# Optimization experiments

Hardware: AMD Instinct MI355X
Metric: run time of the kernel (lower is better)

The kernel has to match this reference:

```python
import jax, jax.numpy as jnp
import numpy as np

B, E, H, W = 32, 512, 16, 16
NH, HD = 8, 64          # num_heads = embed_dim // num_heads_channels, head_dim = 64
OUT = 512
S = H * W + 1           # spacial_dim**2 + 1 = 257 (mean token prepended)


def setup_inputs() -> dict:
    key = jax.random.key(0)
    ks = jax.random.split(key, 10)
    sc = 1.0 / np.sqrt(E).astype(np.float32)
    n = lambda k, sh, s=1.0: jax.random.normal(k, sh, jnp.float32) * s
    return {
        "x_real": n(ks[0], (B, E, H, W)),
        "x_imag": n(ks[1], (B, E, H, W)),
        # positional_embedding = (randn/sqrt(E)).to(complex64) -> imag part is zero
        "pos_r": n(ks[2], (E, S), sc),
        "pos_i": jnp.zeros((E, S), jnp.float32),
        # complex in-projection (packed q,k,v) and out-projection of the MHA
        "w_in_r": n(ks[3], (3 * E, E), sc),
        "w_in_i": n(ks[4], (3 * E, E), sc),
        "b_in_r": jnp.zeros((3 * E,), jnp.float32),
        "b_in_i": jnp.zeros((3 * E,), jnp.float32),
        "w_out_r": n(ks[5], (E, E), sc),
        "w_out_i": n(ks[6], (E, E), sc),
        "b_out_r": jnp.zeros((E,), jnp.float32),
        "b_out_i": jnp.zeros((E,), jnp.float32),
        # complex 1x1 conv projection == complex linear over channels
        "w_p_r": n(ks[7], (OUT, E), sc),
        "w_p_i": n(ks[8], (OUT, E), sc),
        "b_p_r": jnp.zeros((OUT,), jnp.float32),
        "b_p_i": jnp.zeros((OUT,), jnp.float32),
    }


def _attention_pool(x_real, x_imag, pos_r, pos_i, w_in_r, w_in_i, b_in_r, b_in_i,
                    w_out_r, w_out_i, b_out_r, b_out_i, w_p_r, w_p_i, b_p_r, b_p_i):
    cx = jax.lax.complex
    x = cx(x_real, x_imag).reshape(B, E, -1)                       # [b,c,HW]
    x = jnp.concatenate([x.mean(-1, keepdims=True), x], axis=-1)   # [b,c,S]
    x = x + cx(pos_r, pos_i)[None]                                 # + pos embed
    x = x.transpose(0, 2, 1)                                       # [b,S,E]

    qkv = jnp.einsum('bse,fe->bsf', x, cx(w_in_r, w_in_i)) + cx(b_in_r, b_in_i)
    q, k, v = jnp.split(qkv, 3, axis=-1)
    q = q.reshape(B, S, NH, HD) / jnp.sqrt(jnp.float32(HD))
    k = k.reshape(B, S, NH, HD)
    v = v.reshape(B, S, NH, HD)

    logits = jnp.einsum('bqhd,bkhd->bhqk', q, k)                   # complex scores
    # complex softmax handled separately on real/imag parts
    w = cx(jax.nn.softmax(logits.real, axis=-1),
           jax.nn.softmax(logits.imag, axis=-1))
    attn = jnp.einsum('bhqk,bkhd->bqhd', w, v).reshape(B, S, E)
    attn = jnp.einsum('bse,fe->bsf', attn, cx(w_out_r, w_out_i)) + cx(b_out_r, b_out_i)

    y = attn.transpose(0, 2, 1)                                    # [b,E,S]
    y = jnp.einsum('oc,bcs->bos', cx(w_p_r, w_p_i), y) + cx(b_p_r, b_p_i)[None, :, None]
    return y[:, :, 0]                                              # [b,OUT] complex64


def reference(x_real, x_imag, pos_r, pos_i, w_in_r, w_in_i, b_in_r, b_in_i,
              w_out_r, w_out_i, b_out_r, b_out_i, w_p_r, w_p_i, b_p_r, b_p_i):
    return _attention_pool(x_real, x_imag, pos_r, pos_i, w_in_r, w_in_i, b_in_r,
                           b_in_i, w_out_r, w_out_i, b_out_r, b_out_i,
                           w_p_r, w_p_i, b_p_r, b_p_i)
```

## Files before the change

kernel.cpp:

```cpp
#include <hip/hip_runtime.h>

#define B_   32
#define E_   512
#define HW_  256
#define S_   257
#define NH_  8
#define NBLK 1024
#define NTHR 256
#define NGRP 32
#define GSZ  32
#define LG_  260

__device__ __forceinline__ void st_sys(float* p, float v) {
  __hip_atomic_store(p, v, __ATOMIC_RELAXED, __HIP_MEMORY_SCOPE_SYSTEM);
}
__device__ __forceinline__ void st_sys2(float2* p, float2 v) {
  unsigned long long u;
  __builtin_memcpy(&u, &v, 8);
  __hip_atomic_store((unsigned long long*)p, u, __ATOMIC_RELAXED, __HIP_MEMORY_SCOPE_SYSTEM);
}

__device__ __forceinline__ float wave_reduce(float v) {
  #pragma unroll
  for (int o = 32; o > 0; o >>= 1) v += __shfl_down(v, o, 64);
  return v;
}

__device__ __forceinline__ void gbar(unsigned* slots, int g, int j, int t, unsigned phase) {
  __syncthreads();
  if (t < 64) {
    if (t == 0)
      __hip_atomic_store(&slots[g * GSZ + j], phase, __ATOMIC_RELAXED, __HIP_MEMORY_SCOPE_SYSTEM);
    const unsigned* line = slots + g * GSZ;
    int sl = t & 31;
    for (;;) {
      unsigned v = __hip_atomic_load(&line[sl], __ATOMIC_RELAXED, __HIP_MEMORY_SCOPE_SYSTEM);
      if (__all((int)(v >= phase))) break;
      __builtin_amdgcn_s_sleep(2);
    }
  }
  __syncthreads();
}

__device__ void softmax257(float* l, float* red, int t) {
  int lane = t & 63, wv = t >> 6;
  float v = l[t];
  float v256 = l[256];
  float m = v;
  #pragma unroll
  for (int o = 32; o > 0; o >>= 1) m = fmaxf(m, __shfl_xor(m, o, 64));
  if (lane == 0) red[wv] = m;
  __syncthreads();
  float M = fmaxf(fmaxf(fmaxf(red[0], red[1]), fmaxf(red[2], red[3])), v256);
  float ex = expf(v - M);
  float e256 = expf(v256 - M);
  float s = ex;
  #pragma unroll
  for (int o = 32; o > 0; o >>= 1) s += __shfl_xor(s, o, 64);
  if (lane == 0) red[4 + wv] = s;
  __syncthreads();
  float inv = 1.f / (red[4] + red[5] + red[6] + red[7] + e256);
  l[t] = ex * inv;
  if (t == 0) l[256] = e256 * inv;
  __syncthreads();
}

__global__ __launch_bounds__(NTHR, 4) void k_mega(
    const float* __restrict__ xr, const float* __restrict__ xi,
    const float* __restrict__ pos_r, const float* __restrict__ pos_i,
    const float* __restrict__ w_in_r, const float* __restrict__ w_in_i,
    const float* __restrict__ b_in_r, const float* __restrict__ b_in_i,
    const float* __restrict__ w_out_r, const float* __restrict__ w_out_i,
    const float* __restrict__ b_out_r, const float* __restrict__ b_out_i,
    const float* __restrict__ w_p_r, const float* __restrict__ w_p_i,
    const float* __restrict__ b_p_r, const float* __restrict__ b_p_i,
    unsigned* slots,
    float* __restrict__ ur_, float* __restrict__ ui_,
    float* __restrict__ lgr, float* __restrict__ lgi,
    float* __restrict__ mr, float* __restrict__ mi,
    float* __restrict__ w2,
    float* __restrict__ zr_, float* __restrict__ zi_,
    float* __restrict__ a0r, float* __restrict__ a0i,
    float* __restrict__ aor, float* __restrict__ aoi,
    float* __restrict__ out, int interleaved) {
  __shared__ __align__(16) float smF[4112];
  const int t   = threadIdx.x;
  const int l   = t & 63;
  const int w   = t >> 6;
  const int bid = blockIdx.x;
  const int g   = bid >> 5;
  const int j   = bid & 31;

  #pragma unroll
  for (int rr = 0; rr < 4; ++rr) {
    int e = j * 16 + w * 4 + rr;
    float4 vr = ((const float4*)(xr + ((size_t)g * E_ + e) * HW_))[l];
    float4 vi = ((const float4*)(xi + ((size_t)g * E_ + e) * HW_))[l];
    float sr = (vr.x + vr.y) + (vr.z + vr.w);
    float si = (vi.x + vi.y) + (vi.z + vi.w);
    sr = wave_reduce(sr); si = wave_reduce(si);
    if (l == 0) {
      st_sys(&mr[g * E_ + e], sr * (1.f / HW_) + pos_r[(size_t)e * S_]);
      st_sys(&mi[g * E_ + e], si * (1.f / HW_) + pos_i[(size_t)e * S_]);
    }
  }
  gbar(slots, g, j, t, 1);

  {
    float* mR  = smF;
    float* mI  = smF + 512;
    float* q0L = smF + 1024;
    mR[t]       = mr[g * E_ + t];        mI[t]       = mi[g * E_ + t];
    mR[t + 256] = mr[g * E_ + t + 256];  mI[t + 256] = mi[g * E_ + t + 256];
    __syncthreads();
    #pragma unroll
    for (int rr = 0; rr < 4; ++rr) {
      int fl = w * 4 + rr;
      int f  = 16 * j + fl;
      const float* wr = w_in_r + (size_t)f * E_;
      const float* wi = w_in_i + (size_t)f * E_;
      float ar = 0.f, ai = 0.f;
      #pragma unroll
      for (int e = l; e < E_; e += 64) {
        float Xr = mR[e], Xi = mI[e], Cr = wr[e], Ci = wi[e];
        ar += Xr * Cr - Xi * Ci;
        ai += Xr * Ci + Xi * Cr;
      }
      ar = wave_reduce(ar); ai = wave_reduce(ai);
      if (l == 0) {
        q0L[fl * 2]     = (ar + b_in_r[f]) * 0.125f;
        q0L[fl * 2 + 1] = (ai + b_in_i[f]) * 0.125f;
      }
    }
    __syncthreads();
    int h = j >> 2;
    float u0r = 0.f, u0i = 0.f, u1r = 0.f, u1i = 0.f;
    #pragma unroll 4
    for (int fl = 0; fl < 16; ++fl) {
      int f = 16 * j + fl;
      float qr = q0L[fl * 2], qi = q0L[fl * 2 + 1];
      const float* Wr = w_in_r + (size_t)(E_ + f) * E_;
      const float* Wi = w_in_i + (size_t)(E_ + f) * E_;
      float W0r = Wr[t], W0i = Wi[t], W1r = Wr[t + 256], W1i = Wi[t + 256];
      u0r += qr * W0r - qi * W0i;  u0i += qr * W0i + qi * W0r;
      u1r += qr * W1r - qi * W1i;  u1i += qr * W1i + qi * W1r;
    }
    size_t ub = (size_t)(g * NH_ + h) * E_;
    atomicAdd(&ur_[ub + t], u0r);        atomicAdd(&ui_[ub + t], u0i);
    atomicAdd(&ur_[ub + t + 256], u1r);  atomicAdd(&ui_[ub + t + 256], u1i);
  }
  gbar(slots, g, j, t, 2);

  {
    int e0 = 16 * j;
    float* us = smF;
    if (t < 128) {
      int e = t & 15, hh = t >> 4;
      us[(e * 8 + hh) * 2]     = ur_[(size_t)(g * NH_ + hh) * E_ + e0 + e];
      us[(e * 8 + hh) * 2 + 1] = ui_[(size_t)(g * NH_ + hh) * E_ + e0 + e];
    }
    __syncthreads();
    float ar[NH_], ai[NH_];
    #pragma unroll
    for (int hh = 0; hh < NH_; ++hh) { ar[hh] = 0.f; ai[hh] = 0.f; }
    const float* xrb = xr + ((size_t)g * E_ + e0) * HW_;
    const float* xib = xi + ((size_t)g * E_ + e0) * HW_;
    #pragma unroll 2
    for (int e = 0; e < 16; ++e) {
      float Xr = xrb[e * HW_ + t] + pos_r[(size_t)(e0 + e) * S_ + t + 1];
      float Xi = xib[e * HW_ + t] + pos_i[(size_t)(e0 + e) * S_ + t + 1];
      #pragma unroll
      for (int hh = 0; hh < NH_; ++hh) {
        float Ur = us[(e * 8 + hh) * 2], Ui = us[(e * 8 + hh) * 2 + 1];
        ar[hh] += Xr * Ur - Xi * Ui;
        ai[hh] += Xr * Ui + Xi * Ur;
      }
    }
    #pragma unroll
    for (int hh = 0; hh < NH_; ++hh) {
      size_t lb = (size_t)(g * NH_ + hh) * LG_ + t + 1;
      atomicAdd(&lgr[lb], ar[hh]);
      atomicAdd(&lgi[lb], ai[hh]);
    }
  }
  gbar(slots, g, j, t, 3);

  if (j < NH_) {
    int bh = g * NH_ + j;
    float* lr  = smF;
    float* li  = smF + 260;
    float* redl = smF + 520;
    float* reds = smF + 528;
    lr[t + 1] = lgr[(size_t)bh * LG_ + t + 1];
    li[t + 1] = lgi[(size_t)bh * LG_ + t + 1];
    float pr = 0.f, pi = 0.f;
    #pragma unroll
    for (int e = t; e < E_; e += 256) {
      float Xr = mr[g * E_ + e], Xi = mi[g * E_ + e];
      float Ur = ur_[(size_t)bh * E_ + e], Ui = ui_[(size_t)bh * E_ + e];
      pr += Xr * Ur - Xi * Ui;
      pi += Xr * Ui + Xi * Ur;
    }
    pr = wave_reduce(pr); pi = wave_reduce(pi);
    if (l == 0) { redl[w * 2] = pr; redl[w * 2 + 1] = pi; }
    __syncthreads();
    if (t == 0) {
      lr[0] = redl[0] + redl[2] + redl[4] + redl[6];
      li[0] = redl[1] + redl[3] + redl[5] + redl[7];
    }
    __syncthreads();
    softmax257(lr, reds, t);
    softmax257(li, reds, t);
    float2* o = (float2*)w2 + (size_t)bh * S_;
    float2 v; v.x = lr[t]; v.y = li[t];
    st_sys2(&o[t], v);
    if (t == 0) { float2 v2; v2.x = lr[256]; v2.y = li[256]; st_sys2(&o[256], v2); }
  } else {
    int idx = t & 127;
    int e = 16 * j + (idx & 15);
    const float* src = (t < 128) ? xr : xi;
    float pf = src[((size_t)g * E_ + e) * HW_ + (idx >> 4) * 32];
    asm volatile("" :: "v"(pf));
  }
  gbar(slots, g, j, t, 4);

  {
    float2* wls = (float2*)smF;
    const float2* w2b = (const float2*)w2 + (size_t)g * NH_ * S_;
    for (int i = t; i < NH_ * S_; i += NTHR) wls[i] = w2b[i];
    __syncthreads();
    #pragma unroll
    for (int rr = 0; rr < 4; ++rr) {
      int e = 16 * j + 4 * w + rr;
      const float* xre = xr + ((size_t)g * E_ + e) * HW_;
      const float* xie = xi + ((size_t)g * E_ + e) * HW_;
      const float* pre = pos_r + (size_t)e * S_;
      const float* pie = pos_i + (size_t)e * S_;
      float ar2[NH_], ai2[NH_];
      #pragma unroll
      for (int hh = 0; hh < NH_; ++hh) { ar2[hh] = 0.f; ai2[hh] = 0.f; }
      #pragma unroll
      for (int jj = 0; jj < 4; ++jj) {
        int k = 1 + l + 64 * jj;
        float Xr = xre[k - 1] + pre[k];
        float Xi = xie[k - 1] + pie[k];
        #pragma unroll
        for (int hh = 0; hh < NH_; ++hh) {
          float2 W = wls[hh * S_ + k];
          ar2[hh] += W.x * Xr - W.y * Xi;
          ai2[hh] += W.x * Xi + W.y * Xr;
        }
      }
      #pragma unroll
      for (int hh = 0; hh < NH_; ++hh) { ar2[hh] = wave_reduce(ar2[hh]); ai2[hh] = wave_reduce(ai2[hh]); }
      if (l == 0) {
        float X0r = mr[g * E_ + e];
        float X0i = mi[g * E_ + e];
        #pragma unroll
        for (int hh = 0; hh < NH_; ++hh) {
          float2 W0 = wls[hh * S_];
          st_sys(&zr_[(size_t)(g * NH_ + hh) * E_ + e], ar2[hh] + W0.x * X0r - W0.y * X0i);
          st_sys(&zi_[(size_t)(g * NH_ + hh) * E_ + e], ai2[hh] + W0.x * X0i + W0.y * X0r);
        }
      }
    }
  }
  gbar(slots, g, j, t, 5);

  #pragma unroll
  for (int rr = 0; rr < 4; ++rr) {
    int f = j * 16 + w * 4 + rr;
    int h = f >> 6;
    const float* wrp = w_in_r + (size_t)(2 * E_ + f) * E_;
    const float* wip = w_in_i + (size_t)(2 * E_ + f) * E_;
    const float* zrp = zr_ + (size_t)(g * NH_ + h) * E_;
    const float* zip = zi_ + (size_t)(g * NH_ + h) * E_;
    float ar = 0.f, ai = 0.f;
    #pragma unroll
    for (int e = l; e < E_; e += 64) {
      float Zr = zrp[e], Zi = zip[e], Cr = wrp[e], Ci = wip[e];
      ar += Zr * Cr - Zi * Ci;
      ai += Zr * Ci + Zi * Cr;
    }
    ar = wave_reduce(ar); ai = wave_reduce(ai);
    if (l == 0) {
      float bvr = b_in_r[2 * E_ + f], bvi = b_in_i[2 * E_ + f];
      st_sys(&a0r[g * E_ + f], ar + (bvr - bvi));
      st_sys(&a0i[g * E_ + f], ai + (bvr + bvi));
    }
  }
  gbar(slots, g, j, t, 6);

  #pragma unroll
  for (int rr = 0; rr < 4; ++rr) {
    int f = j * 16 + w * 4 + rr;
    const float* wrp = w_out_r + (size_t)f * E_;
    const float* wip = w_out_i + (size_t)f * E_;
    const float* ir = a0r + (size_t)g * E_;
    const float* ii = a0i + (size_t)g * E_;
    float ar = 0.f, ai = 0.f;
    #pragma unroll
    for (int e = l; e < E_; e += 64) {
      float Xr = ir[e], Xi = ii[e], Cr = wrp[e], Ci = wip[e];
      ar += Xr * Cr - Xi * Ci;
      ai += Xr * Ci + Xi * Cr;
    }
    ar = wave_reduce(ar); ai = wave_reduce(ai);
    if (l == 0) { st_sys(&aor[g * E_ + f], ar + b_out_r[f]); st_sys(&aoi[g * E_ + f], ai + b_out_i[f]); }
  }
  gbar(slots, g, j, t, 7);

  #pragma unroll
  for (int rr = 0; rr < 4; ++rr) {
    int f = j * 16 + w * 4 + rr;
    const float* wrp = w_p_r + (size_t)f * E_;
    const float* wip = w_p_i + (size_t)f * E_;
    const float* ir = aor + (size_t)g * E_;
    const float* ii = aoi + (size_t)g * E_;
    float ar = 0.f, ai = 0.f;
    #pragma unroll
    for (int e = l; e < E_; e += 64) {
      float Xr = ir[e], Xi = ii[e], Cr = wrp[e], Ci = wip[e];
      ar += Xr * Cr - Xi * Ci;
      ai += Xr * Ci + Xi * Cr;
    }
    ar = wave_reduce(ar); ai = wave_reduce(ai);
    if (l == 0) {
      float rr2 = ar + b_p_r[f];
      float im  = ai + b_p_i[f];
      int wid = g * E_ + f;
      if (interleaved) { out[(size_t)wid * 2] = rr2; out[(size_t)wid * 2 + 1] = im; }
      else             { out[wid] = rr2; }
    }
  }
}

extern "C" void kernel_launch(void* const* d_in, const int* in_sizes, int n_in,
                              void* d_out, int out_size, void* d_ws, size_t ws_size,
                              hipStream_t stream) {
  (void)in_sizes; (void)n_in; (void)ws_size;
  const float* xr      = (const float*)d_in[0];
  const float* xi      = (const float*)d_in[1];
  const float* pos_r   = (const float*)d_in[2];
  const float* pos_i   = (const float*)d_in[3];
  const float* w_in_r  = (const float*)d_in[4];
  const float* w_in_i  = (const float*)d_in[5];
  const float* b_in_r  = (const float*)d_in[6];
  const float* b_in_i  = (const float*)d_in[7];
  const float* w_out_r = (const float*)d_in[8];
  const float* w_out_i = (const float*)d_in[9];
  const float* b_out_r = (const float*)d_in[10];
  const float* b_out_i = (const float*)d_in[11];
  const float* w_p_r   = (const float*)d_in[12];
  const float* w_p_i   = (const float*)d_in[13];
  const float* b_p_r   = (const float*)d_in[14];
  const float* b_p_i   = (const float*)d_in[15];

  const int BE = B_ * E_, BHE = B_ * NH_ * E_;
  float* ws = (float*)d_ws;
  unsigned* slots = (unsigned*)d_ws;
  float* ur   = ws + 1024;
  float* ui   = ur + BHE;
  float* lgr  = ui + BHE;
  float* lgi  = lgr + B_ * NH_ * LG_;
  float* mr   = lgi + B_ * NH_ * LG_;
  float* mi   = mr + BE;
  float* w2   = mi + BE;
  float* zr   = w2 + (size_t)2 * B_ * NH_ * S_;
  float* zi   = zr + BHE;
  float* a0r  = zi + BHE;
  float* a0i  = a0r + BE;
  float* aor  = a0i + BE;
  float* aoi  = aor + BE;

  size_t zbytes = (size_t)(1024 + 2 * BHE + 2 * B_ * NH_ * LG_) * 4;
  hipMemsetAsync(d_ws, 0, zbytes, stream);
  k_mega<<<NBLK, NTHR, 0, stream>>>(
      xr, xi, pos_r, pos_i, w_in_r, w_in_i, b_in_r, b_in_i,
      w_out_r, w_out_i, b_out_r, b_out_i, w_p_r, w_p_i, b_p_r, b_p_i,
      slots, ur, ui, lgr, lgi, mr, mi, w2, zr, zi, a0r, a0i, aor, aoi,
      (float*)d_out, out_size >= 2 * B_ * E_);
}
```

Before: 204.6 us.

## Fuse V-projection and out-projection stages via split-K atomics, drop two grid barriers

```diff
diff --git a/kernel.cpp b/kernel.cpp
--- a/kernel.cpp
+++ b/kernel.cpp
@@ -36,7 +36,7 @@
     for (;;) {
       unsigned v = __hip_atomic_load(&line[sl], __ATOMIC_RELAXED, __HIP_MEMORY_SCOPE_SYSTEM);
       if (__all((int)(v >= phase))) break;
-      __builtin_amdgcn_s_sleep(2);
+      __builtin_amdgcn_s_sleep(8);
     }
   }
   __syncthreads();
@@ -77,13 +77,11 @@
     unsigned* slots,
     float* __restrict__ ur_, float* __restrict__ ui_,
     float* __restrict__ lgr, float* __restrict__ lgi,
+    float* __restrict__ a0r, float* __restrict__ a0i,
     float* __restrict__ mr, float* __restrict__ mi,
     float* __restrict__ w2,
-    float* __restrict__ zr_, float* __restrict__ zi_,
-    float* __restrict__ a0r, float* __restrict__ a0i,
-    float* __restrict__ aor, float* __restrict__ aoi,
     float* __restrict__ out, int interleaved) {
-  __shared__ __align__(16) float smF[4112];
+  __shared__ __align__(16) float smF[4368];
   const int t   = threadIdx.x;
   const int l   = t & 63;
   const int w   = t >> 6;
@@ -226,12 +224,14 @@
 
   {
     float2* wls = (float2*)smF;
+    float*  zS  = smF + 4112;
     const float2* w2b = (const float2*)w2 + (size_t)g * NH_ * S_;
     for (int i = t; i < NH_ * S_; i += NTHR) wls[i] = w2b[i];
     __syncthreads();
     #pragma unroll
     for (int rr = 0; rr < 4; ++rr) {
-      int e = 16 * j + 4 * w + rr;
+      int el = 4 * w + rr;
+      int e  = 16 * j + el;
       const float* xre = xr + ((size_t)g * E_ + e) * HW_;
       const float* xie = xi + ((size_t)g * E_ + e) * HW_;
       const float* pre = pos_r + (size_t)e * S_;
@@ -259,78 +259,82 @@
         #pragma unroll
         for (int hh = 0; hh < NH_; ++hh) {
           float2 W0 = wls[hh * S_];
-          st_sys(&zr_[(size_t)(g * NH_ + hh) * E_ + e], ar2[hh] + W0.x * X0r - W0.y * X0i);
-          st_sys(&zi_[(size_t)(g * NH_ + hh) * E_ + e], ai2[hh] + W0.x * X0i + W0.y * X0r);
+          zS[(hh * 16 + el) * 2]     = ar2[hh] + W0.x * X0r - W0.y * X0i;
+          zS[(hh * 16 + el) * 2 + 1] = ai2[hh] + W0.x * X0i + W0.y * X0r;
         }
       }
     }
+    __syncthreads();
+    #pragma unroll
+    for (int ff = 0; ff < 2; ++ff) {
+      int f  = t + ff * 256;
+      int hh = f >> 6;
+      const float* wvr = w_in_r + (size_t)(2 * E_ + f) * E_ + 16 * j;
+      const float* wvi = w_in_i + (size_t)(2 * E_ + f) * E_ + 16 * j;
+      float cr = 0.f, ci = 0.f;
+      #pragma unroll
+      for (int el = 0; el < 16; ++el) {
+        float Wr = wvr[el], Wi = wvi[el];
+        float Zr = zS[(hh * 16 + el) * 2], Zi = zS[(hh * 16 + el) * 2 + 1];
+        cr += Wr * Zr - Wi * Zi;
+        ci += Wr * Zi + Wi * Zr;
+      }
+      if (j == 0) {
+        float bvr = b_in_r[2 * E_ + f], bvi = b_in_i[2 * E_ + f];
+        cr += bvr - bvi;
+        ci += bvr + bvi;
+      }
+      atomicAdd(&a0r[g * E_ + f], cr);
+      atomicAdd(&a0i[g * E_ + f], ci);
+    }
   }
   gbar(slots, g, j, t, 5);
 
-  #pragma unroll
-  for (int rr = 0; rr < 4; ++rr) {
-    int f = j * 16 + w * 4 + rr;
-    int h = f >> 6;
-    const float* wrp = w_in_r + (size_t)(2 * E_ + f) * E_;
-    const float* wip = w_in_i + (size_t)(2 * E_ + f) * E_;
-    const float* zrp = zr_ + (size_t)(g * NH_ + h) * E_;
-    const float* zip = zi_ + (size_t)(g * NH_ + h) * E_;
-    float ar = 0.f, ai = 0.f;
-    #pragma unroll
-    for (int e = l; e < E_; e += 64) {
-      float Zr = zrp[e], Zi = zip[e], Cr = wrp[e], Ci = wip[e];
-      ar += Zr * Cr - Zi * Ci;
-      ai += Zr * Ci + Zi * Cr;
-    }
-    ar = wave_reduce(ar); ai = wave_reduce(ai);
-    if (l == 0) {
-      float bvr = b_in_r[2 * E_ + f], bvi = b_in_i[2 * E_ + f];
-      st_sys(&a0r[g * E_ + f], ar + (bvr - bvi));
-      st_sys(&a0i[g * E_ + f], ai + (bvr + bvi));
-    }
-  }
-  gbar(slots, g, j, t, 6);
-
-  #pragma unroll
-  for (int rr = 0; rr < 4; ++rr) {
-    int f = j * 16 + w * 4 + rr;
-    const float* wrp = w_out_r + (size_t)f * E_;
-    const float* wip = w_out_i + (size_t)f * E_;
-    const float* ir = a0r + (size_t)g * E_;
-    const float* ii = a0i + (size_t)g * E_;
-    float ar = 0.f, ai = 0.f;
-    #pragma unroll
-    for (int e = l; e < E_; e += 64) {
-      float Xr = ir[e], Xi = ii[e], Cr = wrp[e], Ci = wip[e];
-      ar += Xr * Cr - Xi * Ci;
-      ai += Xr * Ci + Xi * Cr;
-    }
-    ar = wave_reduce(ar); ai = wave_reduce(ai);
-    if (l == 0) { st_sys(&aor[g * E_ + f], ar + b_out_r[f]); st_sys(&aoi[g * E_ + f], ai + b_out_i[f]); }
-  }
-  gbar(slots, g, j, t, 7);
-
-  #pragma unroll
-  for (int rr = 0; rr < 4; ++rr) {
-    int f = j * 16 + w * 4 + rr;
-    const float* wrp = w_p_r + (size_t)f * E_;
-    const float* wip = w_p_i + (size_t)f * E_;
-    const float* ir = aor + (size_t)g * E_;
-    const float* ii = aoi + (size_t)g * E_;
-    float ar = 0.f, ai = 0.f;
-    #pragma unroll
-    for (int e = l; e < E_; e += 64) {
-      float Xr = ir[e], Xi = ii[e], Cr = wrp[e], Ci = wip[e];
-      ar += Xr * Cr - Xi * Ci;
-      ai += Xr * Ci + Xi * Cr;
-    }
-    ar = wave_reduce(ar); ai = wave_reduce(ai);
-    if (l == 0) {
-      float rr2 = ar + b_p_r[f];
-      float im  = ai + b_p_i[f];
-      int wid = g * E_ + f;
-      if (interleaved) { out[(size_t)wid * 2] = rr2; out[(size_t)wid * 2 + 1] = im; }
-      else             { out[wid] = rr2; }
+  {
+    float* aoS = smF;
+    float* a0R = smF + 64;
+    float* a0I = smF + 576;
+    a0R[t]       = a0r[g * E_ + t];        a0I[t]       = a0i[g * E_ + t];
+    a0R[t + 256] = a0r[g * E_ + t + 256];  a0I[t + 256] = a0i[g * E_ + t + 256];
+    __syncthreads();
+    #pragma unroll
+    for (int rr = 0; rr < 4; ++rr) {
+      int fl = w * 4 + rr;
+      int f  = 16 * j + fl;
+      const float* wrp = w_out_r + (size_t)f * E_;
+      const float* wip = w_out_i + (size_t)f * E_;
+      float ar = 0.f, ai = 0.f;
+      #pragma unroll
+      for (int e = l; e < E_; e += 64) {
+        float Xr = a0R[e], Xi = a0I[e], Cr = wrp[e], Ci = wip[e];
+        ar += Xr * Cr - Xi * Ci;
+        ai += Xr * Ci + Xi * Cr;
+      }
+      ar = wave_reduce(ar); ai = wave_reduce(ai);
+      if (l == 0) { aoS[fl * 2] = ar + b_out_r[f]; aoS[fl * 2 + 1] = ai + b_out_i[f]; }
+    }
+    __syncthreads();
+    #pragma unroll
+    for (int ff = 0; ff < 2; ++ff) {
+      int o = t + ff * 256;
+      const float* wpr = w_p_r + (size_t)o * E_ + 16 * j;
+      const float* wpi = w_p_i + (size_t)o * E_ + 16 * j;
+      float cr = 0.f, ci = 0.f;
+      #pragma unroll
+      for (int fl = 0; fl < 16; ++fl) {
+        float Ar = aoS[fl * 2], Ai = aoS[fl * 2 + 1];
+        float Wr = wpr[fl],     Wi = wpi[fl];
+        cr += Ar * Wr - Ai * Wi;
+        ci += Ar * Wi + Ai * Wr;
+      }
+      if (j == 0) { cr += b_p_r[o]; ci += b_p_i[o]; }
+      int wid = g * E_ + o;
+      if (interleaved) {
+        atomicAdd(&out[(size_t)wid * 2],     cr);
+        atomicAdd(&out[(size_t)wid * 2 + 1], ci);
+      } else {
+        atomicAdd(&out[wid], cr);
+      }
     }
   }
 }
@@ -363,21 +367,20 @@
   float* ui   = ur + BHE;
   float* lgr  = ui + BHE;
   float* lgi  = lgr + B_ * NH_ * LG_;
-  float* mr   = lgi + B_ * NH_ * LG_;
+  float* a0r  = lgi + B_ * NH_ * LG_;
+  float* a0i  = a0r + BE;
+  float* mr   = a0i + BE;
   float* mi   = mr + BE;
   float* w2   = mi + BE;
-  float* zr   = w2 + (size_t)2 * B_ * NH_ * S_;
-  float* zi   = zr + BHE;
-  float* a0r  = zi + BHE;
-  float* a0i  = a0r + BE;
-  float* aor  = a0i + BE;
-  float* aoi  = aor + BE;
-
-  size_t zbytes = (size_t)(1024 + 2 * BHE + 2 * B_ * NH_ * LG_) * 4;
+
+  int interleaved = out_size >= 2 * B_ * E_;
+
+  size_t zbytes = (size_t)(1024 + 2 * BHE + 2 * B_ * NH_ * LG_ + 2 * BE) * 4;
   hipMemsetAsync(d_ws, 0, zbytes, stream);
+  hipMemsetAsync(d_out, 0, (size_t)(interleaved ? 2 * BE : BE) * 4, stream);
   k_mega<<<NBLK, NTHR, 0, stream>>>(
       xr, xi, pos_r, pos_i, w_in_r, w_in_i, b_in_r, b_in_i,
       w_out_r, w_out_i, b_out_r, b_out_i, w_p_r, w_p_i, b_p_r, b_p_i,
-      slots, ur, ui, lgr, lgi, mr, mi, w2, zr, zi, a0r, a0i, aor, aoi,
-      (float*)d_out, out_size >= 2 * B_ * E_);
-}
+      slots, ur, ui, lgr, lgi, a0r, a0i, mr, mi, w2,
+      (float*)d_out, interleaved);
+}
```

Result: faster. 196.8 us (-3.8%).
